# Kernel optimization log

Hardware: AMD Instinct MI355X
Metric: run time of the kernel (lower is better)

The kernel has to match this reference:

```python
import jax, jax.numpy as jnp
import numpy as np

N = 4_194_304  # total points
C = 2          # classes: 0=ground, 1=plant
B = 8          # number of point clouds in the batch
SIGMA_L = 0.1
SIGMA_R = 0.4
CLAMP_FACTOR = 2.0
MIN_VAL = 0.1
FOCAL_GAMMA = 2.0
FOCAL_ALPHA = 1.0
LOSS_WEIGHT = 1.0


def setup_inputs() -> dict:
    key = jax.random.key(0)
    k1, k2, k3 = jax.random.split(key, 3)
    pred = jax.random.normal(k1, (N, C), dtype=jnp.float32)
    coord = jax.random.normal(k2, (N, 3), dtype=jnp.float32)
    segment = jax.random.randint(k3, (N,), 0, C, dtype=jnp.int32)
    # pointcept-style cumulative offsets: equal-sized clouds, offset[-1] == N
    offset = (jnp.arange(1, B + 1, dtype=jnp.int32) * (N // B))
    return {"pred": pred, "coord": coord, "segment": segment, "offset": offset}


def _gauss_weights(z, segment, batch):
    # per-cloud z_ground_max (fallback: z.min) and z_plant_min (fallback: z.max)
    neg_inf = jnp.array(-jnp.inf, z.dtype)
    pos_inf = jnp.array(jnp.inf, z.dtype)
    gmax = jax.ops.segment_max(jnp.where(segment == 0, z, neg_inf), batch, num_segments=B)
    pmin = jax.ops.segment_min(jnp.where(segment == 1, z, pos_inf), batch, num_segments=B)
    has_g = jax.ops.segment_sum((segment == 0).astype(z.dtype), batch, num_segments=B) > 0
    has_p = jax.ops.segment_sum((segment == 1).astype(z.dtype), batch, num_segments=B) > 0
    zmin = jax.ops.segment_min(z, batch, num_segments=B)
    zmax = jax.ops.segment_max(z, batch, num_segments=B)
    g = jnp.where(has_g, gmax, zmin)
    p = jnp.where(has_p, pmin, zmax)
    mu_b = g + (p - g) * 0.5  # (B,)
    mu = mu_b[batch]          # (N,)
    d = z - mu
    w_left = jnp.exp(-(d * d) / (2.0 * SIGMA_L * SIGMA_L))
    w_right = jnp.exp(-(d * d) / (2.0 * SIGMA_R * SIGMA_R))
    w_right = jnp.where(d > CLAMP_FACTOR * SIGMA_R, jnp.array(MIN_VAL, z.dtype), w_right)
    return jnp.where(z <= mu, w_left, w_right)


def reference(pred, coord, segment, offset):
    n = pred.shape[0]
    # offset2batch: per-point batch id from cumulative offsets
    batch = jnp.searchsorted(offset, jnp.arange(n, dtype=offset.dtype), side='right')
    # cross entropy (reduction='none')
    logp = jax.nn.log_softmax(pred, axis=1)              # (N, C)
    logp_t = jnp.take_along_axis(logp, segment[:, None], axis=1)[:, 0]  # (N,)
    seg_loss = (-logp_t) * LOSS_WEIGHT
    # focal reweighting (computed under no_grad in the original)
    p_t = jax.lax.stop_gradient(jnp.exp(logp_t))
    focal_weight = FOCAL_ALPHA * (1.0 - p_t) ** FOCAL_GAMMA
    seg_loss = seg_loss * focal_weight
    # asymmetric gaussian z-weighting, segment-conditioned per cloud
    weights = _gauss_weights(coord[:, 2], segment, batch)
    return jnp.mean(seg_loss * weights)
```

## Files before the change

### kernel.cpp

```cpp
#include <hip/hip_runtime.h>
#include <math.h>

#define THREADS 256
#define NBLOCKS 256
#define ROUNDS  8
#define U       8
#define CHUNK   (ROUNDS * U * THREADS)

__device__ __forceinline__ unsigned enc_f(float f) {
    unsigned b = __float_as_uint(f);
    return (b & 0x80000000u) ? ~b : (b | 0x80000000u);
}
__device__ __forceinline__ float dec_f(unsigned u) {
    unsigned b = (u & 0x80000000u) ? (u ^ 0x80000000u) : ~u;
    return __uint_as_float(b);
}
#define ENC_NEG_INF 0x007FFFFFu
#define ENC_POS_INF 0xFF800000u


__global__ void k_init(unsigned* __restrict__ ws) {
    int t = threadIdx.x;
    if (t < 32) ws[t] = (t < 8 || t >= 24) ? ENC_NEG_INF : ENC_POS_INF;
    else if (t == 32) { *(double*)(ws + 32) = 0.0; ws[34] = 0u; ws[35] = 0u; }
}

#define CNT_B(ii, bdst) do { bdst = 0; \
    _Pragma("unroll") for (int j_ = 0; j_ < 8; ++j_) bdst += ((ii) >= roff[j_]); } while (0)

#define FLUSH_G(bb, g_, p_, mn_, mx_) do { \
    atomicMax(&ws[      (bb)], enc_f(g_));  \
    atomicMin(&ws[ 8  + (bb)], enc_f(p_));  \
    atomicMin(&ws[16  + (bb)], enc_f(mn_)); \
    atomicMax(&ws[24  + (bb)], enc_f(mx_)); } while (0)

__device__ __forceinline__ float point_loss(float p0, float p1, int s, float z, float mu) {
    float m   = fmaxf(p0, p1);
    float lse = m + logf(expf(p0 - m) + expf(p1 - m));
    float lpt = ((s == 0) ? p0 : p1) - lse;
    float pt  = expf(lpt);
    float om  = 1.0f - pt;
    float loss = -lpt * om * om;
    float d  = z - mu;
    float cf = (z <= mu) ? 50.0f : 3.125f;
    float w  = expf(-d * d * cf);
    if (z > mu && d > 0.8f) w = 0.1f;
    return loss * w;
}

__global__ __launch_bounds__(THREADS) void k_fused(
        const float* __restrict__ pred, const float* __restrict__ coord,
        const int* __restrict__ segment, const int* __restrict__ offset,
        unsigned* __restrict__ ws, float* __restrict__ out, int n, int nb) {
    __shared__ float    s_mu[8];
    __shared__ float    s_part[THREADS / 64];
    __shared__ unsigned s_raw[32];
    const int tid = threadIdx.x;
    int roff[8];
    #pragma unroll
    for (int j = 0; j < 8; ++j) roff[j] = (j < nb) ? offset[j] : 0x7FFFFFFF;

    const int chunk = (n + (int)gridDim.x - 1) / (int)gridDim.x;
    const int start = blockIdx.x * chunk;
    const int end   = min(n, start + chunk);

    int ba = 0, bz = 0;
    if (start < end) {
        #pragma unroll
        for (int j = 0; j < 8; ++j) { ba += (start >= roff[j]); bz += ((end - 1) >= roff[j]); }
    }
    const bool fast = (start < end) && (ba == bz) && (end - start == CHUNK) && (chunk == CHUNK);

    float zc[ROUNDS][U];
    unsigned long long segb = 0ull;
    float lg = -INFINITY, lp = INFINITY, lmn = INFINITY, lmx = -INFINITY;

    if (fast) {
        #pragma unroll
        for (int r = 0; r < ROUNDS; ++r) {
            const int base = start + tid + r * U * THREADS;
            int sk[U];
            #pragma unroll
            for (int k = 0; k < U; ++k) zc[r][k] = coord[3 * (base + k * THREADS) + 2];
            #pragma unroll
            for (int k = 0; k < U; ++k) sk[k] = segment[base + k * THREADS];
            #pragma unroll
            for (int k = 0; k < U; ++k) {
                const float z = zc[r][k];
                lmn = fminf(lmn, z); lmx = fmaxf(lmx, z);
                lg  = fmaxf(lg, (sk[k] == 0) ? z : -INFINITY);
                lp  = fminf(lp, (sk[k] != 0) ? z : INFINITY);
                segb |= ((unsigned long long)(sk[k] & 1)) << (r * U + k);
            }
        }
        #pragma unroll
        for (int m = 32; m; m >>= 1) {
            lg  = fmaxf(lg,  __shfl_xor(lg,  m, 64));
            lp  = fminf(lp,  __shfl_xor(lp,  m, 64));
            lmn = fminf(lmn, __shfl_xor(lmn, m, 64));
            lmx = fmaxf(lmx, __shfl_xor(lmx, m, 64));
        }
        if ((tid & 63) == 0) FLUSH_G(ba, lg, lp, lmn, lmx);
    } else if (start < end) {
        int curb = -1;
        for (int i = start + tid; i < end; i += THREADS) {
            float z = coord[3 * i + 2]; int s = segment[i], b;
            CNT_B(i, b);
            if (b != curb) {
                if (curb >= 0) FLUSH_G(curb, lg, lp, lmn, lmx);
                lg = -INFINITY; lp = INFINITY; lmn = INFINITY; lmx = -INFINITY;
                curb = b;
            }
            lmn = fminf(lmn, z); lmx = fmaxf(lmx, z);
            if (s == 0) lg = fmaxf(lg, z); else lp = fminf(lp, z);
        }
        if (curb >= 0) FLUSH_G(curb, lg, lp, lmn, lmx);
    }

    __syncthreads();
    if (tid == 0) {
        atomicAdd(&ws[35], 1u);
        int tries = 1 << 22;
        while (atomicAdd(&ws[35], 0u) < (unsigned)gridDim.x && --tries)
            __builtin_amdgcn_s_sleep(8);
        __threadfence();
    }
    __syncthreads();

    if (tid < 32) s_raw[tid] = atomicOr(&ws[tid], 0u);
    __syncthreads();
    if (tid < 8) {
        unsigned ug = s_raw[tid], up = s_raw[8 + tid];
        float g = dec_f(ug), p = dec_f(up);
        if (ug == ENC_NEG_INF) g = dec_f(s_raw[16 + tid]);
        if (up == ENC_POS_INF) p = dec_f(s_raw[24 + tid]);
        s_mu[tid] = g + (p - g) * 0.5f;
    }
    __syncthreads();

    float lsum = 0.0f;
    const float2* pred2 = (const float2*)pred;
    if (fast) {
        const float mu = s_mu[ba];
        #pragma unroll
        for (int r = 0; r < ROUNDS; ++r) {
            const int base = start + tid + r * U * THREADS;
            float2 pp[U];
            #pragma unroll
            for (int k = 0; k < U; ++k) pp[k] = pred2[base + k * THREADS];
            #pragma unroll
            for (int k = 0; k < U; ++k)
                lsum += point_loss(pp[k].x, pp[k].y,
                                   (int)((segb >> (r * U + k)) & 1ull), zc[r][k], mu);
        }
    } else if (start < end) {
        for (int i = start + tid; i < end; i += THREADS) {
            int b; CNT_B(i, b);
            float2 pp = pred2[i];
            lsum += point_loss(pp.x, pp.y, segment[i], coord[3 * i + 2], s_mu[b]);
        }
    }

    #pragma unroll
    for (int off = 32; off > 0; off >>= 1) lsum += __shfl_down(lsum, off, 64);
    if ((tid & 63) == 0) s_part[tid >> 6] = lsum;
    __syncthreads();
    if (tid == 0) {
        float t = 0.0f;
        #pragma unroll
        for (int wv = 0; wv < THREADS / 64; ++wv) t += s_part[wv];
        double* acc = (double*)(ws + 32);
        atomicAdd(acc, (double)t);
        __threadfence();
        unsigned c = atomicAdd(&ws[34], 1u);
        if (c == (unsigned)gridDim.x - 1u) {
            double v = atomicAdd(acc, 0.0);
            out[0] = (float)(v / (double)n);
        }
    }
}

extern "C" void kernel_launch(void* const* d_in, const int* in_sizes, int n_in,
                              void* d_out, int out_size, void* d_ws, size_t ws_size,
                              hipStream_t stream) {
    const float* pred    = (const float*)d_in[0];
    const float* coord   = (const float*)d_in[1];
    const int*   segment = (const int*)d_in[2];
    const int*   offset  = (const int*)d_in[3];
    const int n  = in_sizes[2];
    const int nb = in_sizes[3];

    unsigned* ws = (unsigned*)d_ws;

    hipLaunchKernelGGL(k_init,  dim3(1), dim3(64), 0, stream, ws);
    hipLaunchKernelGGL(k_fused, dim3(NBLOCKS), dim3(THREADS), 0, stream,
                       pred, coord, segment, offset, ws, (float*)d_out, n, nb);
}
```

Baseline: 161.3 us.

## Quadruple threads per block and stash cached z values in LDS

Each block grows from 256 to 1024 threads and each thread now handles 16 points instead of 64. The per-thread z cache moves from a register array into a shared-memory buffer, and the segment bitmask shrinks to 32 bits. With one block per CU, this gives more waves per CU and more loads in flight for this latency-bound reduction and loss pass. The price is a large static LDS allocation and a slightly retuned grid-barrier spin (extra fence, shorter sleep, more tries).

```diff
diff --git a/kernel.cpp b/kernel.cpp
--- a/kernel.cpp
+++ b/kernel.cpp
@@ -1,11 +1,11 @@
 #include <hip/hip_runtime.h>
 #include <math.h>
 
-#define THREADS 256
+#define THREADS 1024
 #define NBLOCKS 256
-#define ROUNDS  8
+#define PTS     16
 #define U       8
-#define CHUNK   (ROUNDS * U * THREADS)
+#define CHUNK   (PTS * THREADS)
 
 __device__ __forceinline__ unsigned enc_f(float f) {
     unsigned b = __float_as_uint(f);
@@ -52,6 +52,7 @@
         const float* __restrict__ pred, const float* __restrict__ coord,
         const int* __restrict__ segment, const int* __restrict__ offset,
         unsigned* __restrict__ ws, float* __restrict__ out, int n, int nb) {
+    __shared__ float    zbuf[24 * THREADS];
     __shared__ float    s_mu[8];
     __shared__ float    s_part[THREADS / 64];
     __shared__ unsigned s_raw[32];
@@ -69,28 +70,27 @@
         #pragma unroll
         for (int j = 0; j < 8; ++j) { ba += (start >= roff[j]); bz += ((end - 1) >= roff[j]); }
     }
-    const bool fast = (start < end) && (ba == bz) && (end - start == CHUNK) && (chunk == CHUNK);
-
-    float zc[ROUNDS][U];
-    unsigned long long segb = 0ull;
+    const bool fast = (start < end) && (ba == bz) && (end - start == chunk) && (chunk == CHUNK);
+
+    unsigned segb = 0u;
     float lg = -INFINITY, lp = INFINITY, lmn = INFINITY, lmx = -INFINITY;
 
     if (fast) {
         #pragma unroll
-        for (int r = 0; r < ROUNDS; ++r) {
+        for (int r = 0; r < PTS / U; ++r) {
             const int base = start + tid + r * U * THREADS;
-            int sk[U];
-            #pragma unroll
-            for (int k = 0; k < U; ++k) zc[r][k] = coord[3 * (base + k * THREADS) + 2];
-            #pragma unroll
-            for (int k = 0; k < U; ++k) sk[k] = segment[base + k * THREADS];
+            float z[U]; int s[U];
+            #pragma unroll
+            for (int k = 0; k < U; ++k) z[k] = coord[3 * (base + k * THREADS) + 2];
+            #pragma unroll
+            for (int k = 0; k < U; ++k) s[k] = segment[base + k * THREADS];
             #pragma unroll
             for (int k = 0; k < U; ++k) {
-                const float z = zc[r][k];
-                lmn = fminf(lmn, z); lmx = fmaxf(lmx, z);
-                lg  = fmaxf(lg, (sk[k] == 0) ? z : -INFINITY);
-                lp  = fminf(lp, (sk[k] != 0) ? z : INFINITY);
-                segb |= ((unsigned long long)(sk[k] & 1)) << (r * U + k);
+                zbuf[(r * U + k) * THREADS + tid] = z[k];
+                segb |= (unsigned)(s[k] & 1) << (r * U + k);
+                lmn = fminf(lmn, z[k]); lmx = fmaxf(lmx, z[k]);
+                lg  = fmaxf(lg, (s[k] == 0) ? z[k] : -INFINITY);
+                lp  = fminf(lp, (s[k] != 0) ? z[k] : INFINITY);
             }
         }
         #pragma unroll
@@ -119,10 +119,11 @@
 
     __syncthreads();
     if (tid == 0) {
+        __threadfence();
         atomicAdd(&ws[35], 1u);
-        int tries = 1 << 22;
+        int tries = 1 << 24;
         while (atomicAdd(&ws[35], 0u) < (unsigned)gridDim.x && --tries)
-            __builtin_amdgcn_s_sleep(8);
+            __builtin_amdgcn_s_sleep(4);
         __threadfence();
     }
     __syncthreads();
@@ -143,15 +144,17 @@
     if (fast) {
         const float mu = s_mu[ba];
         #pragma unroll
-        for (int r = 0; r < ROUNDS; ++r) {
+        for (int r = 0; r < PTS / U; ++r) {
             const int base = start + tid + r * U * THREADS;
-            float2 pp[U];
+            float2 pp[U]; float z[U];
             #pragma unroll
             for (int k = 0; k < U; ++k) pp[k] = pred2[base + k * THREADS];
+            #pragma unroll
+            for (int k = 0; k < U; ++k) z[k] = zbuf[(r * U + k) * THREADS + tid];
             #pragma unroll
             for (int k = 0; k < U; ++k)
                 lsum += point_loss(pp[k].x, pp[k].y,
-                                   (int)((segb >> (r * U + k)) & 1ull), zc[r][k], mu);
+                                   (int)((segb >> (r * U + k)) & 1u), z[k], mu);
         }
     } else if (start < end) {
         for (int i = start + tid; i < end; i += THREADS) {
```

Result: slower. 233.8 us (+45.0%).
